# Kernel tuning notes

Measured on AMD Instinct MI355X. Metric: run time of the kernel, lower is better.

## Reference

```python
import jax, jax.numpy as jnp
import numpy as np

B, T, D = 4, 8192, 1024
C = 8.0


def setup_inputs() -> dict:
    key = jax.random.key(0)
    k1, k2, k3 = jax.random.split(key, 3)
    init_std = D ** (-0.5)
    x = jax.random.normal(k1, (B, T, D), dtype=jnp.float32)
    W_in = jax.random.truncated_normal(k2, -3.0, 3.0, (D, D), dtype=jnp.float32) * init_std
    W_gate = jax.random.truncated_normal(k3, -3.0, 3.0, (D, D), dtype=jnp.float32) * init_std
    b_in = jnp.zeros((D,), dtype=jnp.float32)
    b_gate = jnp.zeros((D,), dtype=jnp.float32)
    forget_lambda = jnp.linspace(-4.323, -9.0, D, dtype=jnp.float32)
    return {"x": x, "W_in": W_in, "b_in": b_in, "W_gate": W_gate,
            "b_gate": b_gate, "forget_lambda": forget_lambda}


def _combine(c1, c2):
    # linear recurrence h_t = a_t * h_{t-1} + b_t  (associative composition)
    a1, b1 = c1
    a2, b2 = c2
    return a1 * a2, a2 * b1 + b2


def reference(x, W_in, b_in, W_gate, b_gate, forget_lambda):
    # x: [B, T, D]
    input_gate = x @ W_in.T + b_in          # [B, T, D]
    recurrence_gate = x @ W_gate.T + b_gate  # [B, T, D]
    alpha = jnp.exp(-C * jax.nn.softplus(forget_lambda) * jax.nn.sigmoid(recurrence_gate))
    beta = jnp.sqrt(1.0 - alpha ** 2 + 1e-6)
    xbeta = beta * jax.nn.sigmoid(input_gate) * x
    # parallel scan of h_t = alpha_t * h_{t-1} + xbeta_t along sequence axis
    _, h = jax.lax.associative_scan(_combine, (alpha, xbeta), axis=1)
    return h
```

## Files before the change

kernel.cpp:

```cpp
#include <hip/hip_runtime.h>

typedef unsigned short u16;
typedef __attribute__((ext_vector_type(8))) short short8;
typedef __attribute__((ext_vector_type(4))) float f32x4;

#define T_SEQ 8192
#define DDIM 1024
#define BB 4
#define MM (BB * T_SEQ)
#define NC 128
#define CHUNK (T_SEQ / NC)
#define CHAINS (BB * DDIM)

__device__ __forceinline__ float bf_lo(unsigned p) {
    union { unsigned u; float f; } v; v.u = p << 16; return v.f;
}
__device__ __forceinline__ float bf_hi(unsigned p) {
    union { unsigned u; float f; } v; v.u = p & 0xffff0000u; return v.f;
}
__device__ __forceinline__ float bf_u16(u16 p) {
    union { unsigned u; float f; } v; v.u = ((unsigned)p) << 16; return v.f;
}
__device__ __forceinline__ u16 f2bf(float f) {
    union { unsigned u; float f; } v; v.f = f;
    unsigned r = v.u + 0x7fffu + ((v.u >> 16) & 1u);
    return (u16)(r >> 16);
}
__device__ __forceinline__ float sigm(float z) {
    return __builtin_amdgcn_rcpf(1.0f + __expf(-z));
}
__device__ __forceinline__ void gld16(const u16* g, u16* l) {
    __builtin_amdgcn_global_load_lds((const __attribute__((address_space(1))) void*)g,
                                     (__attribute__((address_space(3))) void*)l, 16, 0, 0);
}

#define N4X (MM * DDIM / 4)
#define N4W (DDIM * DDIM / 4)
__global__ __launch_bounds__(256) void cvt_all(const float* __restrict__ x,
                                               const float* __restrict__ Wi,
                                               const float* __restrict__ Wg,
                                               u16* __restrict__ Xb,
                                               u16* __restrict__ Wib,
                                               u16* __restrict__ Wgb) {
    int i = blockIdx.x * 256 + threadIdx.x;
    const float* src; u16* dst; int j;
    if (i < N4X)            { src = x;  dst = Xb;  j = i; }
    else if (i < N4X + N4W) { src = Wi; dst = Wib; j = i - N4X; }
    else                    { src = Wg; dst = Wgb; j = i - N4X - N4W; }
    float4 v = ((const float4*)src)[j];
    ushort4 o;
    o.x = f2bf(v.x); o.y = f2bf(v.y); o.z = f2bf(v.z); o.w = f2bf(v.w);
    ((ushort4*)dst)[j] = o;
}


#define MROWJ(i_, av, J)                                                                     \
    acc[i_][(J)+0] = __builtin_amdgcn_mfma_f32_16x16x32_bf16(av, b0, acc[i_][(J)+0], 0,0,0); \
    acc[i_][(J)+1] = __builtin_amdgcn_mfma_f32_16x16x32_bf16(av, b1, acc[i_][(J)+1], 0,0,0); \
    acc[i_][(J)+2] = __builtin_amdgcn_mfma_f32_16x16x32_bf16(av, b2, acc[i_][(J)+2], 0,0,0); \
    acc[i_][(J)+3] = __builtin_amdgcn_mfma_f32_16x16x32_bf16(av, b3, acc[i_][(J)+3], 0,0,0);

#define MQUADJ(J) MROWJ(0, a0, J) MROWJ(1, a1, J) MROWJ(2, a2, J) MROWJ(3, a3, J)

#define LDA_S(s_, i) (*(const short8*)&lds[(s_)*4096 + (arow0 + (i)*16)*32 + aoff])
#define LDB_S(s_, j) (*(const short8*)&lds[12288 + (s_)*8192 + (brow0 + (j)*16)*32 + aoff])

#define STA_R(s_, ht_, rb) gld16(gA + (size_t)(ht_)*32 + (size_t)(rb)*64*DDIM,               \
                                 &lds[(s_)*4096 + (rb)*2048 + tid*8])
#define STB_R(s_, ht_, rb) gld16(((rb) < 2 ? gBi + (size_t)(rb)*64*DDIM                      \
                                           : gBg + (size_t)((rb)-2)*64*DDIM)                 \
                                     + (size_t)(ht_)*32,                                     \
                                 &lds[12288 + (s_)*8192 + (rb)*2048 + tid*8])

#define PAIRX(s_, ss_, ht_, DOST, VMS)                                                       \
                                                                           \
    b0 = LDB_S(s_, 0); b1 = LDB_S(s_, 1); b2 = LDB_S(s_, 2); b3 = LDB_S(s_, 3);              \
    a0 = LDA_S(s_, 0); a1 = LDA_S(s_, 1); a2 = LDA_S(s_, 2); a3 = LDA_S(s_, 3);              \
    if (DOST) { STA_R(ss_, ht_, 0); STA_R(ss_, ht_, 1); STB_R(ss_, ht_, 0); }                \
    __builtin_amdgcn_s_barrier();                                                            \
    asm volatile("s_waitcnt lgkmcnt(0)" ::: "memory");                                       \
    __builtin_amdgcn_sched_barrier(0);                                                       \
    __builtin_amdgcn_s_setprio(1);                                                           \
    MQUADJ(0)                                                                                \
    __builtin_amdgcn_s_setprio(0);                                                           \
    __builtin_amdgcn_s_barrier();                                                            \
                                                                           \
    b0 = LDB_S(s_, 4); b1 = LDB_S(s_, 5); b2 = LDB_S(s_, 6); b3 = LDB_S(s_, 7);              \
    if (DOST) { STB_R(ss_, ht_, 1); STB_R(ss_, ht_, 2); STB_R(ss_, ht_, 3); }                \
    asm volatile("s_waitcnt " VMS ::: "memory");                                             \
    __builtin_amdgcn_s_barrier();                                                            \
    asm volatile("s_waitcnt lgkmcnt(0)" ::: "memory");                                       \
    __builtin_amdgcn_sched_barrier(0);                                                       \
    __builtin_amdgcn_s_setprio(1);                                                           \
    MQUADJ(4)                                                                                \
    __builtin_amdgcn_s_setprio(0);                                                           \
    __builtin_amdgcn_s_barrier();

__global__ __launch_bounds__(256, 2)
void gemm_fused(const u16* __restrict__ X, const u16* __restrict__ Wi,
                const u16* __restrict__ Wg, const float* __restrict__ b_in,
                const float* __restrict__ b_gate, const float* __restrict__ lam,
                u16* __restrict__ Sg, u16* __restrict__ XBg,
                float* __restrict__ AggA, float* __restrict__ AggB) {
    const int bid = blockIdx.x;
    const int xcd = bid & 7;
    const int r = bid >> 3;
    const int n_tile = r & 7;
    const int m_tile = xcd * 32 + (r >> 3);
    const int tN0 = n_tile * 128;
    const int tM0 = m_tile * 128;

    const int tid = threadIdx.x;
    const int lane = tid & 63;
    const int w = tid >> 6;
    const int wm = w & 1;
    const int gate = w >> 1;

    __shared__ u16 lds[36864];

    const int srow = tid >> 2;
    const int c8log = (tid & 3) ^ ((tid >> 3) & 3);
    const u16* gA  = X  + (size_t)(tM0 + srow) * DDIM + c8log * 8;
    const u16* gBi = Wi + (size_t)(tN0 + srow) * DDIM + c8log * 8;
    const u16* gBg = Wg + (size_t)(tN0 + srow) * DDIM + c8log * 8;

    const int lm = lane & 15;
    const int aoff = (((lane >> 4) ^ ((lm >> 1) & 3))) * 8;
    const int arow0 = wm * 64 + lm;
    const int brow0 = gate * 128 + lm;

    f32x4 acc[4][8] = {};
    short8 a0, a1, a2, a3, b0, b1, b2, b3;

    STA_R(0, 0, 0); STA_R(0, 0, 1); STB_R(0, 0, 0); STB_R(0, 0, 1); STB_R(0, 0, 2); STB_R(0, 0, 3);
    STA_R(1, 1, 0); STA_R(1, 1, 1); STB_R(1, 1, 0); STB_R(1, 1, 1); STB_R(1, 1, 2); STB_R(1, 1, 3);
    asm volatile("s_waitcnt vmcnt(6)" ::: "memory");
    __builtin_amdgcn_s_barrier();

    for (int g = 0; g < 10; ++g) {
        const int hb = 3 * g;
        PAIRX(0, 2, hb + 2, 1, "vmcnt(6)")
        PAIRX(1, 0, hb + 3, 1, "vmcnt(6)")
        PAIRX(2, 1, hb + 4, 1, "vmcnt(6)")
    }
    PAIRX(0, 0, 0, 0, "vmcnt(0)")
    PAIRX(1, 0, 0, 0, "vmcnt(0)")

    const int r0 = (lane >> 4) << 2;
    const int cb = lane & 15;
    if (gate) {
#pragma unroll
        for (int j = 0; j < 8; ++j) {
            const int colg = tN0 + j * 16 + cb;
            const int cl = j * 16 + cb;
            const float bj = b_gate[colg];
            const float nsp = -8.0f * log1pf(__expf(lam[colg]));
#pragma unroll
            for (int i = 0; i < 4; ++i) {
                const int rl0 = wm * 64 + i * 16 + r0;
#pragma unroll
                for (int rr = 0; rr < 4; ++rr) {
                    const int rl = rl0 + rr;
                    float s = nsp * sigm(acc[i][j][rr] + bj);
                    lds[rl * 128 + (cl ^ (((rl >> 2) & 7) << 4))] = f2bf(s);
                }
            }
        }
    } else {
#pragma unroll
        for (int j = 0; j < 8; ++j) {
            const int colg = tN0 + j * 16 + cb;
            const int cl = j * 16 + cb;
            const float bj = b_in[colg];
#pragma unroll
            for (int i = 0; i < 4; ++i) {
                const int rl0 = wm * 64 + i * 16 + r0;
#pragma unroll
                for (int rr = 0; rr < 4; ++rr) {
                    const int rl = rl0 + rr;
                    float p = sigm(acc[i][j][rr] + bj);
                    lds[16384 + rl * 128 + (cl ^ (((rl >> 2) & 7) << 4))] =
                        (u16)(p * 65535.0f + 0.5f);
                }
            }
        }
    }
    asm volatile("s_waitcnt lgkmcnt(0)" ::: "memory");
    __builtin_amdgcn_s_barrier();
    __builtin_amdgcn_sched_barrier(0);

    const int cc = tid & 15;
    const int rg0 = (tid >> 4) * 8;
    float Aacc[8] = {1.f, 1.f, 1.f, 1.f, 1.f, 1.f, 1.f, 1.f};
    float Bacc[8] = {};
#pragma unroll
    for (int k = 0; k < 8; ++k) {
        const int rl = rg0 + k;
        const int ch = (cc ^ (((rl >> 2) & 7) << 1)) * 8;
        short8 sv = *(const short8*)&lds[rl * 128 + ch];
        short8 pv = *(const short8*)&lds[16384 + rl * 128 + ch];
        const size_t go = (size_t)(tM0 + rl) * DDIM + tN0 + cc * 8;
        short8 xv = *(const short8*)&X[go];
        short8 ov;
#pragma unroll
        for (int e = 0; e < 8; ++e) {
            float s = bf_u16((u16)sv[e]);
            float p = (float)((u16)pv[e]) * (1.0f / 65535.0f);
            float xf = bf_u16((u16)xv[e]);
            float be = sqrtf(1.0f - __expf(2.0f * s) + 1e-6f);
            u16 xbq = f2bf(be * p * xf);
            ov[e] = (short)xbq;
            float a = __expf(s);
            Bacc[e] = fmaf(a, Bacc[e], bf_u16(xbq));
            Aacc[e] *= a;
        }
        *(short8*)&Sg[go] = sv;
        *(short8*)&XBg[go] = ov;
    }

    asm volatile("s_waitcnt lgkmcnt(0)" ::: "memory");
    __builtin_amdgcn_s_barrier();
    {
        float* fA = (float*)lds;
        float* fB = (float*)lds + 2048;
        const int seg = tid >> 4;
#pragma unroll
        for (int e = 0; e < 8; ++e) {
            fA[seg * 128 + cc * 8 + e] = Aacc[e];
            fB[seg * 128 + cc * 8 + e] = Bacc[e];
        }
        asm volatile("s_waitcnt lgkmcnt(0)" ::: "memory");
        __builtin_amdgcn_s_barrier();
        const int chk = tid >> 7;
        const int col = tid & 127;
        float A = 1.0f, Bv = 0.0f;
#pragma unroll
        for (int k = 0; k < 8; ++k) {
            float a = fA[(chk * 8 + k) * 128 + col];
            float b = fB[(chk * 8 + k) * 128 + col];
            Bv = fmaf(a, Bv, b);
            A *= a;
        }
        const int bq = tM0 >> 13;
        const int cw = ((tM0 & 8191) >> 6) + chk;
        const size_t gi = (size_t)cw * CHAINS + bq * DDIM + tN0 + col;
        AggA[gi] = A;
        AggB[gi] = Bv;
    }
}

__global__ __launch_bounds__(256)
void scan_pass2(const float* __restrict__ AggA, const float* __restrict__ AggB,
                float* __restrict__ H0) {
    const int chain = blockIdx.x * 256 + threadIdx.x;
    float p = 0.0f;
#pragma unroll 8
    for (int c = 0; c < NC; c++) {
        H0[(size_t)c * CHAINS + chain] = p;
        p = AggA[(size_t)c * CHAINS + chain] * p + AggB[(size_t)c * CHAINS + chain];
    }
}

__global__ __launch_bounds__(256)
void scan_pass3(const u16* __restrict__ S, const u16* __restrict__ XB,
                const float* __restrict__ H0, float* __restrict__ out) {
    const int c = blockIdx.x, bq = blockIdx.z;
    const int d0 = threadIdx.x * 4;
    size_t base = ((size_t)(bq * T_SEQ + c * CHUNK)) * DDIM + d0;
    const int chain = bq * DDIM + d0;

    float4 h = *(const float4*)(H0 + (size_t)c * CHAINS + chain);
#pragma unroll 4
    for (int t = 0; t < CHUNK; t++) {
        ushort4 sp = *(const ushort4*)(S + base);
        ushort4 xp = *(const ushort4*)(XB + base);
        h.x = fmaf(__expf(bf_u16(sp.x)), h.x, bf_u16(xp.x));
        h.y = fmaf(__expf(bf_u16(sp.y)), h.y, bf_u16(xp.y));
        h.z = fmaf(__expf(bf_u16(sp.z)), h.z, bf_u16(xp.z));
        h.w = fmaf(__expf(bf_u16(sp.w)), h.w, bf_u16(xp.w));
        *(float4*)(out + base) = h;
        base += DDIM;
    }
}

extern "C" void kernel_launch(void* const* d_in, const int* in_sizes, int n_in,
                              void* d_out, int out_size, void* d_ws, size_t ws_size,
                              hipStream_t stream) {
    const float* x   = (const float*)d_in[0];
    const float* Win = (const float*)d_in[1];
    const float* bin = (const float*)d_in[2];
    const float* Wg  = (const float*)d_in[3];
    const float* bg  = (const float*)d_in[4];
    const float* lam = (const float*)d_in[5];
    float* out = (float*)d_out;

    char* w = (char*)d_ws;
    u16* Wi_bf  = (u16*)(w);
    u16* Wg_bf  = (u16*)(w + (size_t)(2) * 1024 * 1024);
    u16* Sg     = (u16*)(w + (size_t)(4) * 1024 * 1024);
    u16* XBg    = (u16*)(w + (size_t)(68) * 1024 * 1024);
    float* AggA = (float*)(w + (size_t)(132) * 1024 * 1024);
    float* AggB = (float*)(w + (size_t)(134) * 1024 * 1024);
    float* H0   = (float*)(w + (size_t)(136) * 1024 * 1024);

    u16* Xbf = (u16*)d_out;

    cvt_all<<<dim3((N4X + 2 * N4W) / 256), dim3(256), 0, stream>>>(
        x, Win, Wg, Xbf, Wi_bf, Wg_bf);

    gemm_fused<<<dim3((DDIM / 128) * (MM / 128)), dim3(256), 0, stream>>>(
        Xbf, Wi_bf, Wg_bf, bin, bg, lam, Sg, XBg, AggA, AggB);

    scan_pass2<<<dim3(CHAINS / 256), dim3(256), 0, stream>>>(AggA, AggB, H0);
    scan_pass3<<<dim3(NC, 1, BB), dim3(256), 0, stream>>>(Sg, XBg, H0, out);
}
```

Before: 452.0 us.

## Load weight B-fragments directly from global into registers, double-buffered

Weight (B) tiles for the fused two-gate GEMM are no longer staged through LDS. Each wave reads its 8 B fragments straight from global memory into a double-buffered register set one k-step ahead, while only the X (A) tile stays on LDS via global_load_lds. The main loop now runs one MFMA phase per k-step instead of two half-phases, which removes half the barriers and the LDS traffic for B and shrinks the LDS footprint. The cost is much higher register pressure (16 extra short8 values per thread) at 2 waves/SIMD occupancy, and direct global reads of B that may be less coalesced and exposed to latency if the prefetch distance is not enough.

```diff
diff --git a/kernel.cpp b/kernel.cpp
--- a/kernel.cpp
+++ b/kernel.cpp
@@ -12,12 +12,6 @@
 #define CHUNK (T_SEQ / NC)
 #define CHAINS (BB * DDIM)
 
-__device__ __forceinline__ float bf_lo(unsigned p) {
-    union { unsigned u; float f; } v; v.u = p << 16; return v.f;
-}
-__device__ __forceinline__ float bf_hi(unsigned p) {
-    union { unsigned u; float f; } v; v.u = p & 0xffff0000u; return v.f;
-}
 __device__ __forceinline__ float bf_u16(u16 p) {
     union { unsigned u; float f; } v; v.u = ((unsigned)p) << 16; return v.f;
 }
@@ -54,47 +48,43 @@
 }
 
 
-#define MROWJ(i_, av, J)                                                                     \
-    acc[i_][(J)+0] = __builtin_amdgcn_mfma_f32_16x16x32_bf16(av, b0, acc[i_][(J)+0], 0,0,0); \
-    acc[i_][(J)+1] = __builtin_amdgcn_mfma_f32_16x16x32_bf16(av, b1, acc[i_][(J)+1], 0,0,0); \
-    acc[i_][(J)+2] = __builtin_amdgcn_mfma_f32_16x16x32_bf16(av, b2, acc[i_][(J)+2], 0,0,0); \
-    acc[i_][(J)+3] = __builtin_amdgcn_mfma_f32_16x16x32_bf16(av, b3, acc[i_][(J)+3], 0,0,0);
-
-#define MQUADJ(J) MROWJ(0, a0, J) MROWJ(1, a1, J) MROWJ(2, a2, J) MROWJ(3, a3, J)
+#define MROWB(i_, av, Bs)                                                                \
+    acc[i_][0] = __builtin_amdgcn_mfma_f32_16x16x32_bf16(av, Bs[0], acc[i_][0], 0,0,0);  \
+    acc[i_][1] = __builtin_amdgcn_mfma_f32_16x16x32_bf16(av, Bs[1], acc[i_][1], 0,0,0);  \
+    acc[i_][2] = __builtin_amdgcn_mfma_f32_16x16x32_bf16(av, Bs[2], acc[i_][2], 0,0,0);  \
+    acc[i_][3] = __builtin_amdgcn_mfma_f32_16x16x32_bf16(av, Bs[3], acc[i_][3], 0,0,0);  \
+    acc[i_][4] = __builtin_amdgcn_mfma_f32_16x16x32_bf16(av, Bs[4], acc[i_][4], 0,0,0);  \
+    acc[i_][5] = __builtin_amdgcn_mfma_f32_16x16x32_bf16(av, Bs[5], acc[i_][5], 0,0,0);  \
+    acc[i_][6] = __builtin_amdgcn_mfma_f32_16x16x32_bf16(av, Bs[6], acc[i_][6], 0,0,0);  \
+    acc[i_][7] = __builtin_amdgcn_mfma_f32_16x16x32_bf16(av, Bs[7], acc[i_][7], 0,0,0);
+
+#define MALLB(Bs) MROWB(0, a0, Bs) MROWB(1, a1, Bs) MROWB(2, a2, Bs) MROWB(3, a3, Bs)
 
 #define LDA_S(s_, i) (*(const short8*)&lds[(s_)*4096 + (arow0 + (i)*16)*32 + aoff])
-#define LDB_S(s_, j) (*(const short8*)&lds[12288 + (s_)*8192 + (brow0 + (j)*16)*32 + aoff])
-
-#define STA_R(s_, ht_, rb) gld16(gA + (size_t)(ht_)*32 + (size_t)(rb)*64*DDIM,               \
+
+#define STA_R(s_, ht_, rb) gld16(gA + (size_t)(ht_)*32 + (size_t)(rb)*64*DDIM,           \
                                  &lds[(s_)*4096 + (rb)*2048 + tid*8])
-#define STB_R(s_, ht_, rb) gld16(((rb) < 2 ? gBi + (size_t)(rb)*64*DDIM                      \
-                                           : gBg + (size_t)((rb)-2)*64*DDIM)                 \
-                                     + (size_t)(ht_)*32,                                     \
-                                 &lds[12288 + (s_)*8192 + (rb)*2048 + tid*8])
-
-#define PAIRX(s_, ss_, ht_, DOST, VMS)                                                       \
-                                                                           \
-    b0 = LDB_S(s_, 0); b1 = LDB_S(s_, 1); b2 = LDB_S(s_, 2); b3 = LDB_S(s_, 3);              \
-    a0 = LDA_S(s_, 0); a1 = LDA_S(s_, 1); a2 = LDA_S(s_, 2); a3 = LDA_S(s_, 3);              \
-    if (DOST) { STA_R(ss_, ht_, 0); STA_R(ss_, ht_, 1); STB_R(ss_, ht_, 0); }                \
-    __builtin_amdgcn_s_barrier();                                                            \
-    asm volatile("s_waitcnt lgkmcnt(0)" ::: "memory");                                       \
-    __builtin_amdgcn_sched_barrier(0);                                                       \
-    __builtin_amdgcn_s_setprio(1);                                                           \
-    MQUADJ(0)                                                                                \
-    __builtin_amdgcn_s_setprio(0);                                                           \
-    __builtin_amdgcn_s_barrier();                                                            \
-                                                                           \
-    b0 = LDB_S(s_, 4); b1 = LDB_S(s_, 5); b2 = LDB_S(s_, 6); b3 = LDB_S(s_, 7);              \
-    if (DOST) { STB_R(ss_, ht_, 1); STB_R(ss_, ht_, 2); STB_R(ss_, ht_, 3); }                \
-    asm volatile("s_waitcnt " VMS ::: "memory");                                             \
-    __builtin_amdgcn_s_barrier();                                                            \
-    asm volatile("s_waitcnt lgkmcnt(0)" ::: "memory");                                       \
-    __builtin_amdgcn_sched_barrier(0);                                                       \
-    __builtin_amdgcn_s_setprio(1);                                                           \
-    MQUADJ(4)                                                                                \
-    __builtin_amdgcn_s_setprio(0);                                                           \
-    __builtin_amdgcn_s_barrier();
+
+#define RD_BG(dst, k0_) {                                                                \
+    dst[0] = *(const short8*)&gBW[(size_t)( 0*16)*DDIM + (k0_)];                         \
+    dst[1] = *(const short8*)&gBW[(size_t)( 1*16)*DDIM + (k0_)];                         \
+    dst[2] = *(const short8*)&gBW[(size_t)( 2*16)*DDIM + (k0_)];                         \
+    dst[3] = *(const short8*)&gBW[(size_t)( 3*16)*DDIM + (k0_)];                         \
+    dst[4] = *(const short8*)&gBW[(size_t)( 4*16)*DDIM + (k0_)];                         \
+    dst[5] = *(const short8*)&gBW[(size_t)( 5*16)*DDIM + (k0_)];                         \
+    dst[6] = *(const short8*)&gBW[(size_t)( 6*16)*DDIM + (k0_)];                         \
+    dst[7] = *(const short8*)&gBW[(size_t)( 7*16)*DDIM + (k0_)]; }
+
+#define PAIRY(s_, ss_, ht_, kn_, DOST, DORD, BCUR, BNXT)                                 \
+    asm volatile("s_waitcnt vmcnt(8)" ::: "memory");          \
+    __builtin_amdgcn_s_barrier();                                                        \
+    if (DOST) { STA_R(ss_, ht_, 0); STA_R(ss_, ht_, 1); }                                \
+    __builtin_amdgcn_sched_barrier(0);                     \
+    if (DORD) { RD_BG(BNXT, kn_) }                                                       \
+    a0 = LDA_S(s_, 0); a1 = LDA_S(s_, 1); a2 = LDA_S(s_, 2); a3 = LDA_S(s_, 3);          \
+    __builtin_amdgcn_s_setprio(1);                                                       \
+    MALLB(BCUR)                                                                          \
+    __builtin_amdgcn_s_setprio(0);
 
 __global__ __launch_bounds__(256, 2)
 void gemm_fused(const u16* __restrict__ X, const u16* __restrict__ Wi,
@@ -116,35 +106,39 @@
     const int wm = w & 1;
     const int gate = w >> 1;
 
-    __shared__ u16 lds[36864];
+    __shared__ u16 lds[32768];
 
     const int srow = tid >> 2;
     const int c8log = (tid & 3) ^ ((tid >> 3) & 3);
-    const u16* gA  = X  + (size_t)(tM0 + srow) * DDIM + c8log * 8;
-    const u16* gBi = Wi + (size_t)(tN0 + srow) * DDIM + c8log * 8;
-    const u16* gBg = Wg + (size_t)(tN0 + srow) * DDIM + c8log * 8;
+    const u16* gA  = X + (size_t)(tM0 + srow) * DDIM + c8log * 8;
 
     const int lm = lane & 15;
-    const int aoff = (((lane >> 4) ^ ((lm >> 1) & 3))) * 8;
+    const int q8 = (lane >> 4) * 8;
+    const int aoff = ((lane >> 4) ^ ((lm >> 1) & 3)) * 8;
     const int arow0 = wm * 64 + lm;
-    const int brow0 = gate * 128 + lm;
+
+    const u16* gBW = (gate ? Wg : Wi) + (size_t)(tN0 + lm) * DDIM + q8;
 
     f32x4 acc[4][8] = {};
-    short8 a0, a1, a2, a3, b0, b1, b2, b3;
-
-    STA_R(0, 0, 0); STA_R(0, 0, 1); STB_R(0, 0, 0); STB_R(0, 0, 1); STB_R(0, 0, 2); STB_R(0, 0, 3);
-    STA_R(1, 1, 0); STA_R(1, 1, 1); STB_R(1, 1, 0); STB_R(1, 1, 1); STB_R(1, 1, 2); STB_R(1, 1, 3);
-    asm volatile("s_waitcnt vmcnt(6)" ::: "memory");
+    short8 a0, a1, a2, a3;
+    short8 B0[8], B1[8];
+
+    STA_R(0, 0, 0); STA_R(0, 0, 1); STA_R(1, 1, 0); STA_R(1, 1, 1);
+    __builtin_amdgcn_sched_barrier(0);
+    RD_BG(B0, 0)
+
+    for (int g = 0; g < 5; ++g) {
+        const int hb = 6 * g;
+        PAIRY(0, 2, hb + 2, (hb + 1) * 32, 1, 1, B0, B1)
+        PAIRY(1, 0, hb + 3, (hb + 2) * 32, 1, 1, B1, B0)
+        PAIRY(2, 1, hb + 4, (hb + 3) * 32, 1, 1, B0, B1)
+        PAIRY(0, 2, hb + 5, (hb + 4) * 32, 1, 1, B1, B0)
+        PAIRY(1, 0, hb + 6, (hb + 5) * 32, 1, 1, B0, B1)
+        PAIRY(2, 1, hb + 7, (hb + 6) * 32, 1, 1, B1, B0)
+    }
+    PAIRY(0, 0, 0, 31 * 32, 0, 1, B0, B1)
+    PAIRY(1, 0, 0, 0,       0, 0, B1, B0)
     __builtin_amdgcn_s_barrier();
-
-    for (int g = 0; g < 10; ++g) {
-        const int hb = 3 * g;
-        PAIRX(0, 2, hb + 2, 1, "vmcnt(6)")
-        PAIRX(1, 0, hb + 3, 1, "vmcnt(6)")
-        PAIRX(2, 1, hb + 4, 1, "vmcnt(6)")
-    }
-    PAIRX(0, 0, 0, 0, "vmcnt(0)")
-    PAIRX(1, 0, 0, 0, "vmcnt(0)")
 
     const int r0 = (lane >> 4) << 2;
     const int cb = lane & 15;
```

After: 576.6 us. 1.28x slower.
